# Performance work log

Hardware: AMD Instinct MI355X
Metric: run time of the kernel (lower is better)

Reference implementation:

```python
import jax, jax.numpy as jnp
import numpy as np
from jax import lax


def setup_inputs() -> dict:
    key = jax.random.key(0)
    k1, k2 = jax.random.split(key)
    B, C_out, C_in, K, H, W = 16, 128, 128, 3, 64, 64
    features = jax.random.normal(k1, (B, C_in, H, W), dtype=jnp.float32)
    dynamic_kernel = jax.random.normal(k2, (B, C_out, C_in, K, K), dtype=jnp.float32)
    return {"features": features, "dynamic_kernel": dynamic_kernel}


def reference(features, dynamic_kernel):
    # Per-sample dynamic conv. unfold+bmm in torch == cross-correlation (conv2d)
    # with the per-sample kernel; we express it as a vmapped implicit-GEMM conv
    # instead of materializing the (C_in*K*K, H*W) unfold buffer.
    padding = 1

    def conv_one(x, w):  # x: (C_in, H, W), w: (C_out, C_in, K, K)
        return lax.conv_general_dilated(
            x[None],                      # (1, C_in, H, W)
            w,
            window_strides=(1, 1),
            padding=[(padding, padding), (padding, padding)],
            dimension_numbers=("NCHW", "OIHW", "NCHW"),
        )[0]                              # (C_out, H, W)

    return jax.vmap(conv_one)(features, dynamic_kernel)  # (B, C_out, H, W)
```

## Files before the change

### kernel.cpp

```cpp
#include <hip/hip_runtime.h>
#include <stdint.h>

#define BATCH 16
#define CIN   128
#define COUT  128
#define IMG_H 64
#define IMG_W 64
#define HW    4096
#define KTOT  1152
#define XH    66
#define XW    66
#define NCQ   16
#define NSTEPS 18
#define ASTEP 8192
#define BSTEP 8192

typedef __attribute__((ext_vector_type(8))) __bf16 bf16x8;
typedef __attribute__((ext_vector_type(4))) float  f32x4;
typedef __attribute__((address_space(1))) const void* gas_p;
typedef __attribute__((address_space(3))) void*       las_p;

static __device__ __forceinline__ unsigned short f2bf(float f) {
  union { float f; uint32_t u; } c; c.f = f;
  uint32_t r = c.u + 0x7fffu + ((c.u >> 16) & 1u);
  return (unsigned short)(r >> 16);
}

static __device__ __forceinline__ void gload_lds16(const unsigned short* g, unsigned short* l) {
  __builtin_amdgcn_global_load_lds((gas_p)g, (las_p)l, 16, 0, 0);
}

__global__ void prep_fused(const float* __restrict__ x, const float* __restrict__ w,
                           unsigned short* __restrict__ wt4, unsigned short* __restrict__ xpad) {
  const int t = threadIdx.x;
  if (blockIdx.x < BATCH * IMG_H) {
    __shared__ uint32_t tile[64 * 68];
    const int b = blockIdx.x >> 6;
    const int h = blockIdx.x & 63;
    const float* xb = x + (size_t)b * CIN * HW + h * IMG_W;
    uint4* xp4 = (uint4*)xpad;

    const int lane16 = t & 15;
    const int g      = t >> 4;
#pragma unroll
    for (int it = 0; it < 4; ++it) {
      const int ci = it * 32 + g * 2;
      const float4 va = *(const float4*)(xb + (size_t)ci * HW + lane16 * 4);
      const float4 vb = *(const float4*)(xb + (size_t)(ci + 1) * HW + lane16 * 4);
      const float av[4] = {va.x, va.y, va.z, va.w};
      const float bv[4] = {vb.x, vb.y, vb.z, vb.w};
#pragma unroll
      for (int cc = 0; cc < 4; ++cc)
        tile[(lane16 * 4 + cc) * 68 + it * 16 + g] =
            (uint32_t)f2bf(av[cc]) | ((uint32_t)f2bf(bv[cc]) << 16);
    }
    __syncthreads();

    const uint32_t rbase = ((uint32_t)b * XH + h + 1) * NCQ;
#pragma unroll
    for (int it = 0; it < 4; ++it) {
      const int o   = it * 256 + t;
      const int cqg = o >> 6;
      const int wc  = o & 63;
      const uint4 v = *(const uint4*)&tile[wc * 68 + cqg * 4];
      xp4[(rbase + cqg) * XW + wc + 1] = v;
    }
    if (t < 32) {
      const int cqg = t & 15;
      const int col = (t >> 4) ? 65 : 0;
      xp4[(rbase + cqg) * XW + col] = make_uint4(0, 0, 0, 0);
    }
    if (h == 0) {
      const uint32_t r0  = (uint32_t)b * XH * NCQ * XW;
      const uint32_t r65 = ((uint32_t)b * XH + 65) * NCQ * XW;
      for (int i = t; i < NCQ * XW; i += 256) {
        xp4[r0 + i]  = make_uint4(0, 0, 0, 0);
        xp4[r65 + i] = make_uint4(0, 0, 0, 0);
      }
    }
  } else {
    const int idx  = blockIdx.x - BATCH * IMG_H;
    const int b    = idx / NSTEPS;
    const int step = idx % NSTEPS;
    const int khkw = step >> 1;
    const int cib  = (step & 1) << 6;
    const float* wb = w + (size_t)b * COUT * KTOT;
    unsigned short* dst = wt4 + ((size_t)b * NSTEPS + step) * ASTEP;
#pragma unroll
    for (int i = 0; i < 4; ++i) {
      const int c  = i * 256 + t;
      const int cq = c >> 7;
      const int co = c & 127;
      const int ci0 = cib + cq * 8;
      const float* src = wb + (size_t)co * KTOT + (size_t)ci0 * 9 + khkw;
      uint32_t p[4];
#pragma unroll
      for (int e = 0; e < 4; ++e)
        p[e] = (uint32_t)f2bf(src[(2 * e) * 9]) | ((uint32_t)f2bf(src[(2 * e + 1) * 9]) << 16);
      *(uint4*)&dst[(size_t)c * 8] = make_uint4(p[0], p[1], p[2], p[3]);
    }
  }
}

__global__ __launch_bounds__(512, 4) void dynconv_gemm(
    const unsigned short* __restrict__ wt4,
    const unsigned short* __restrict__ xpad,
    float* __restrict__ out) {
  __shared__ alignas(16) unsigned short As[2][ASTEP];
  __shared__ alignas(16) unsigned short Bs[2][BSTEP];

  const int t   = threadIdx.x;
  const int bid = blockIdx.x;
  const int xcd = bid & 7;
  const int idx = bid >> 3;
  const int b   = xcd * 2 + (idx >> 5);
  const int oh0 = (idx & 31) * 2;

  const int lane = t & 63;
  const int wave = t >> 6;
  const int wm   = (wave & 1) << 6;
  const int wn   = (wave >> 1) << 5;
  const int l15  = lane & 15;
  const int quad = lane >> 4;

  const unsigned short* abase = wt4 + (size_t)b * NSTEPS * ASTEP + (size_t)t * 8;
  const unsigned short* xb = xpad + (size_t)b * XH * NCQ * XW * 8;
  const unsigned short* bconst[2];
#pragma unroll
  for (int i = 0; i < 2; ++i)
    bconst[i] = xb + (size_t)((i * NCQ + wave) * XW + lane) * 8;

  unsigned short* alds[2][2];
  unsigned short* blds[2][2];
#pragma unroll
  for (int u = 0; u < 2; ++u) {
#pragma unroll
    for (int r = 0; r < 2; ++r) alds[u][r] = &As[u][(r * 512 + wave * 64) * 8];
#pragma unroll
    for (int i = 0; i < 2; ++i) blds[u][i] = &Bs[u][(wave * 128 + i * 64) * 8];
  }

  f32x4 acc[4][2] = {};

  {
    const size_t boff0 = (size_t)(oh0 * NCQ) * XW * 8;
#pragma unroll
    for (int r = 0; r < 2; ++r) gload_lds16(abase + r * 4096, alds[0][r]);
#pragma unroll
    for (int i = 0; i < 2; ++i) gload_lds16(bconst[i] + boff0, blds[0][i]);
  }
  __syncthreads();

#pragma unroll 2
  for (int step = 0; step < NSTEPS; ++step) {
    const int cur = step & 1;

    if (step + 1 < NSTEPS) {
      const int s2   = step + 1;
      const int khkw = s2 >> 1;
      const int kh   = (khkw * 11) >> 5;
      const int kw   = khkw - kh * 3;
      const size_t boff = ((size_t)((oh0 + kh) * NCQ + ((s2 & 1) << 3)) * XW + kw) * 8;
      const unsigned short* astep = abase + (size_t)s2 * ASTEP;
#pragma unroll
      for (int r = 0; r < 2; ++r) gload_lds16(astep + r * 4096, alds[cur ^ 1][r]);
#pragma unroll
      for (int i = 0; i < 2; ++i) gload_lds16(bconst[i] + boff, blds[cur ^ 1][i]);
    }

#pragma unroll
    for (int ks = 0; ks < 2; ++ks) {
      const int cq = ks * 4 + quad;
      bf16x8 af[4], bf[2];
#pragma unroll
      for (int i = 0; i < 4; ++i)
        af[i] = *(const bf16x8*)&As[cur][(cq * 128 + wm + i * 16 + l15) * 8];
#pragma unroll
      for (int j = 0; j < 2; ++j)
        bf[j] = *(const bf16x8*)&Bs[cur][(cq * 128 + wn + j * 16 + l15) * 8];
#pragma unroll
      for (int i = 0; i < 4; ++i)
#pragma unroll
        for (int j = 0; j < 2; ++j)
          acc[i][j] = __builtin_amdgcn_mfma_f32_16x16x32_bf16(af[i], bf[j], acc[i][j], 0, 0, 0);
    }

    __syncthreads();
  }

  float* obase = out + (size_t)b * COUT * HW + (size_t)oh0 * IMG_W;
#pragma unroll
  for (int i = 0; i < 4; ++i) {
#pragma unroll
    for (int r = 0; r < 4; ++r) {
      const int co = wm + i * 16 + quad * 4 + r;
      float* orow = obase + (size_t)co * HW;
#pragma unroll
      for (int j = 0; j < 2; ++j)
        orow[wn + j * 16 + l15] = acc[i][j][r];
    }
  }
}

__global__ void dynconv_naive(const float* __restrict__ x, const float* __restrict__ w,
                              float* __restrict__ out) {
  const int o   = blockIdx.x * 256 + threadIdx.x;
  const int pix = o & (HW - 1);
  const int co  = (o >> 12) & (COUT - 1);
  const int b   = o >> 19;
  const int oh  = pix >> 6, ow = pix & 63;
  const float* xb = x + (size_t)b * CIN * HW;
  const float* wb = w + ((size_t)b * COUT + co) * CIN * 9;
  float s = 0.f;
  for (int ci = 0; ci < CIN; ++ci) {
    const float* xc = xb + ci * HW;
    const float* wc = wb + ci * 9;
#pragma unroll
    for (int kh = 0; kh < 3; ++kh) {
      const int ih = oh + kh - 1;
      if ((unsigned)ih >= IMG_H) continue;
#pragma unroll
      for (int kw = 0; kw < 3; ++kw) {
        const int iw = ow + kw - 1;
        if ((unsigned)iw >= IMG_W) continue;
        s += xc[ih * IMG_W + iw] * wc[kh * 3 + kw];
      }
    }
  }
  out[o] = s;
}

extern "C" void kernel_launch(void* const* d_in, const int* in_sizes, int n_in,
                              void* d_out, int out_size, void* d_ws, size_t ws_size,
                              hipStream_t stream) {
  const float* x = (const float*)d_in[0];
  const float* w = (const float*)d_in[1];
  float* out = (float*)d_out;

  const size_t wt_bytes = (size_t)BATCH * NSTEPS * ASTEP * sizeof(unsigned short);
  const size_t xp_bytes = (size_t)BATCH * XH * NCQ * XW * 8 * sizeof(unsigned short);

  if (ws_size >= wt_bytes + xp_bytes) {
    unsigned short* wt4  = (unsigned short*)d_ws;
    unsigned short* xpad = (unsigned short*)((char*)d_ws + wt_bytes);
    prep_fused<<<BATCH * IMG_H + BATCH * NSTEPS, 256, 0, stream>>>(x, w, wt4, xpad);
    dynconv_gemm<<<512, 512, 0, stream>>>(wt4, xpad, out);
  } else {
    dynconv_naive<<<(BATCH * COUT * HW) / 256, 256, 0, stream>>>(x, w, out);
  }
}
```

Before: 121.2 us.

## Stage full padded input rows in LDS once and stream only weights per step

Each block now covers 4 output rows instead of 2 and loads all 6 needed padded input rows (all channels) into LDS up front. The main loop then streams only half-steps of the weight tile, double-buffered, so each input element is loaded from global memory once per block instead of once per kernel tap. The block count halves to 256 and the per-wave tile grows to 64x64 with 16 accumulators, which raises register use and LDS footprint and lowers occupancy. The loop also runs 36 smaller steps, each ending in a barrier.

```diff
diff --git a/kernel.cpp b/kernel.cpp
--- a/kernel.cpp
+++ b/kernel.cpp
@@ -13,7 +13,8 @@
 #define NCQ   16
 #define NSTEPS 18
 #define ASTEP 8192
-#define BSTEP 8192
+#define AHALF 4096
+#define NHSTEP 36
 
 typedef __attribute__((ext_vector_type(8))) __bf16 bf16x8;
 typedef __attribute__((ext_vector_type(4))) float  f32x4;
@@ -102,93 +103,82 @@
   }
 }
 
-__global__ __launch_bounds__(512, 4) void dynconv_gemm(
+__global__ __launch_bounds__(512, 2) void dynconv_gemm(
     const unsigned short* __restrict__ wt4,
     const unsigned short* __restrict__ xpad,
     float* __restrict__ out) {
-  __shared__ alignas(16) unsigned short As[2][ASTEP];
-  __shared__ alignas(16) unsigned short Bs[2][BSTEP];
+  __shared__ alignas(16) unsigned short Ah[2][AHALF];
+  __shared__ alignas(16) unsigned short Bp[6][NCQ][XW * 8];
 
   const int t   = threadIdx.x;
   const int bid = blockIdx.x;
   const int xcd = bid & 7;
   const int idx = bid >> 3;
-  const int b   = xcd * 2 + (idx >> 5);
-  const int oh0 = (idx & 31) * 2;
+  const int b   = xcd * 2 + (idx >> 4);
+  const int oh0 = (idx & 15) * 4;
 
   const int lane = t & 63;
   const int wave = t >> 6;
   const int wm   = (wave & 1) << 6;
-  const int wn   = (wave >> 1) << 5;
+  const int prow = wave >> 1;
   const int l15  = lane & 15;
   const int quad = lane >> 4;
 
   const unsigned short* abase = wt4 + (size_t)b * NSTEPS * ASTEP + (size_t)t * 8;
   const unsigned short* xb = xpad + (size_t)b * XH * NCQ * XW * 8;
-  const unsigned short* bconst[2];
-#pragma unroll
-  for (int i = 0; i < 2; ++i)
-    bconst[i] = xb + (size_t)((i * NCQ + wave) * XW + lane) * 8;
-
-  unsigned short* alds[2][2];
-  unsigned short* blds[2][2];
-#pragma unroll
-  for (int u = 0; u < 2; ++u) {
-#pragma unroll
-    for (int r = 0; r < 2; ++r) alds[u][r] = &As[u][(r * 512 + wave * 64) * 8];
-#pragma unroll
-    for (int i = 0; i < 2; ++i) blds[u][i] = &Bs[u][(wave * 128 + i * 64) * 8];
-  }
-
-  f32x4 acc[4][2] = {};
-
-  {
-    const size_t boff0 = (size_t)(oh0 * NCQ) * XW * 8;
-#pragma unroll
-    for (int r = 0; r < 2; ++r) gload_lds16(abase + r * 4096, alds[0][r]);
-#pragma unroll
-    for (int i = 0; i < 2; ++i) gload_lds16(bconst[i] + boff0, blds[0][i]);
-  }
+
+  f32x4 acc[4][4] = {};
+
+#pragma unroll
+  for (int k = 0; k < 12; ++k) {
+    const int p   = wave * 12 + k;
+    const int row = p >> 4;
+    const int cq  = p & 15;
+    const unsigned short* src =
+        xb + ((size_t)((oh0 + row) * NCQ + cq) * XW + (size_t)lane) * 8;
+    unsigned short* dst = &Bp[row][cq][0];
+    gload_lds16(src, dst);
+    gload_lds16(src + 16, dst + 16);
+  }
+  gload_lds16(abase, &Ah[0][wave * 512]);
   __syncthreads();
 
-#pragma unroll 2
-  for (int step = 0; step < NSTEPS; ++step) {
-    const int cur = step & 1;
-
-    if (step + 1 < NSTEPS) {
-      const int s2   = step + 1;
-      const int khkw = s2 >> 1;
-      const int kh   = (khkw * 11) >> 5;
-      const int kw   = khkw - kh * 3;
-      const size_t boff = ((size_t)((oh0 + kh) * NCQ + ((s2 & 1) << 3)) * XW + kw) * 8;
-      const unsigned short* astep = abase + (size_t)s2 * ASTEP;
-#pragma unroll
-      for (int r = 0; r < 2; ++r) gload_lds16(astep + r * 4096, alds[cur ^ 1][r]);
-#pragma unroll
-      for (int i = 0; i < 2; ++i) gload_lds16(bconst[i] + boff, blds[cur ^ 1][i]);
-    }
-
-#pragma unroll
-    for (int ks = 0; ks < 2; ++ks) {
-      const int cq = ks * 4 + quad;
-      bf16x8 af[4], bf[2];
-#pragma unroll
-      for (int i = 0; i < 4; ++i)
-        af[i] = *(const bf16x8*)&As[cur][(cq * 128 + wm + i * 16 + l15) * 8];
-#pragma unroll
-      for (int j = 0; j < 2; ++j)
-        bf[j] = *(const bf16x8*)&Bs[cur][(cq * 128 + wn + j * 16 + l15) * 8];
-#pragma unroll
-      for (int i = 0; i < 4; ++i)
-#pragma unroll
-        for (int j = 0; j < 2; ++j)
-          acc[i][j] = __builtin_amdgcn_mfma_f32_16x16x32_bf16(af[i], bf[j], acc[i][j], 0, 0, 0);
-    }
+#pragma unroll 4
+  for (int h = 0; h < NHSTEP; ++h) {
+    const int u = h & 1;
+
+    if (h + 1 < NHSTEP) {
+      const int h2   = h + 1;
+      const int kk2  = h2 >> 2;
+      const int q42  = h2 & 3;
+      const int stp  = kk2 * 2 + (q42 >> 1);
+      const size_t aoff = (size_t)stp * ASTEP + (size_t)(q42 & 1) * AHALF;
+      gload_lds16(abase + aoff, &Ah[u ^ 1][wave * 512]);
+    }
+
+    const int khkw = h >> 2;
+    const int q4   = h & 3;
+    const int kh   = (khkw * 11) >> 5;
+    const int kw   = khkw - kh * 3;
+
+    bf16x8 af[4], bfr[4];
+#pragma unroll
+    for (int i = 0; i < 4; ++i)
+      af[i] = *(const bf16x8*)&Ah[u][(quad * 128 + wm + i * 16 + l15) * 8];
+#pragma unroll
+    for (int j = 0; j < 4; ++j)
+      bfr[j] = *(const bf16x8*)&Bp[kh + prow][q4 * 4 + quad][(kw + j * 16 + l15) * 8];
+#pragma unroll
+    for (int i = 0; i < 4; ++i)
+#pragma unroll
+      for (int j = 0; j < 4; ++j)
+        acc[i][j] = __builtin_amdgcn_mfma_f32_16x16x32_bf16(af[i], bfr[j], acc[i][j], 0, 0, 0);
 
     __syncthreads();
   }
 
   float* obase = out + (size_t)b * COUT * HW + (size_t)oh0 * IMG_W;
+  const int pxb = prow * 64;
 #pragma unroll
   for (int i = 0; i < 4; ++i) {
 #pragma unroll
@@ -196,8 +186,8 @@
       const int co = wm + i * 16 + quad * 4 + r;
       float* orow = obase + (size_t)co * HW;
 #pragma unroll
-      for (int j = 0; j < 2; ++j)
-        orow[wn + j * 16 + l15] = acc[i][j][r];
+      for (int j = 0; j < 4; ++j)
+        orow[pxb + j * 16 + l15] = acc[i][j][r];
     }
   }
 }
@@ -244,7 +234,7 @@
     unsigned short* wt4  = (unsigned short*)d_ws;
     unsigned short* xpad = (unsigned short*)((char*)d_ws + wt_bytes);
     prep_fused<<<BATCH * IMG_H + BATCH * NSTEPS, 256, 0, stream>>>(x, w, wt4, xpad);
-    dynconv_gemm<<<512, 512, 0, stream>>>(wt4, xpad, out);
+    dynconv_gemm<<<256, 512, 0, stream>>>(wt4, xpad, out);
   } else {
     dynconv_naive<<<(BATCH * COUT * HW) / 256, 256, 0, stream>>>(x, w, out);
   }
```

Measured after the change: 125.8 us. 1.04x slower.
